# Kernel tuning notes

Measured on AMD Instinct MI355X. Metric: run time of the kernel, lower is better.

Reference implementation:

```python
import jax, jax.numpy as jnp
import numpy as np

C = 256      # edge_width
H = 8        # num_heads
D = C // H   # dot dim per head
SCALE = D ** (-0.5)
LN_EPS = 1e-5


def layernorm(x, g, b):
    mu = jnp.mean(x, axis=-1, keepdims=True)
    var = jnp.mean(jnp.square(x - mu), axis=-1, keepdims=True)
    return (x - mu) * jax.lax.rsqrt(var + LN_EPS) * g + b


def setup_inputs() -> dict:
    key = jax.random.key(0)
    ks = jax.random.split(key, 12)
    B, N = 1, 160
    s = 0.02
    return {
        "e": jax.random.normal(ks[0], (B, N, N, C), jnp.float32),
        "mask": jnp.zeros((B, N, N, H), jnp.float32),
        "ln_g": jnp.ones((C,), jnp.float32),
        "ln_b": jnp.zeros((C,), jnp.float32),
        "Wqkv_in": jax.random.normal(ks[1], (C, 3 * C), jnp.float32) * s,
        "bqkv_in": jnp.zeros((3 * C,), jnp.float32),
        "Weg_in": jax.random.normal(ks[2], (C, 2 * H), jnp.float32) * s,
        "beg_in": jnp.zeros((2 * H,), jnp.float32),
        "Wqkv_out": jax.random.normal(ks[3], (C, 3 * C), jnp.float32) * s,
        "bqkv_out": jnp.zeros((3 * C,), jnp.float32),
        "Weg_out": jax.random.normal(ks[4], (C, 2 * H), jnp.float32) * s,
        "beg_out": jnp.zeros((2 * H,), jnp.float32),
        "Wo": jax.random.normal(ks[5], (2 * C, C), jnp.float32) * s,
        "bo": jnp.zeros((C,), jnp.float32),
    }


def reference(e, mask, ln_g, ln_b, Wqkv_in, bqkv_in, Weg_in, beg_in,
              Wqkv_out, bqkv_out, Weg_out, beg_out, Wo, bo):
    B, N, _, _ = e.shape
    e_ln = layernorm(e, ln_g, ln_b)

    def split_qkv(W, b):
        qkv = e_ln @ W + b                       # [B,N,N,3C]
        q, k, v = jnp.split(qkv, 3, axis=-1)
        shp = (B, N, N, D, H)                    # (dot_dim, heads) heads fastest
        return q.reshape(shp) * SCALE, k.reshape(shp), v.reshape(shp)

    # ---- incoming triangle attention ----
    Q_in, K_in, V_in = split_qkv(Wqkv_in, bqkv_in)
    eg_in = (e_ln @ Weg_in + beg_in)[:, :, None, :, :]   # [B,N,1,N,2H]
    E_in, G_in = jnp.split(eg_in, 2, axis=-1)            # each [B,N,1,N,H]
    mask_in = mask[:, :, None]                           # [B,N,1,N,H]
    H_in = jnp.einsum('bijdh,bjkdh->bijkh', Q_in, K_in) + E_in
    A_in = jax.nn.softmax(H_in + mask_in, axis=3) * jax.nn.sigmoid(G_in + mask_in)
    Va_in = jnp.einsum('bijkh,bjkdh->bijdh', A_in, V_in)

    # ---- outgoing triangle attention ----
    Q_out, K_out, V_out = split_qkv(Wqkv_out, bqkv_out)
    eg_out = (e_ln @ Weg_out + beg_out)[:, :, :, None, :]  # [B,N,N,1,2H]
    E_out, G_out = jnp.split(eg_out, 2, axis=-1)           # each [B,N,N,1,H]
    mask_out = mask[:, :, :, None]                         # [B,N,N,1,H]
    H_out = jnp.einsum('bijdh,bkjdh->bkijh', Q_out, K_out) + E_out
    A_out = jax.nn.softmax(H_out + mask_out, axis=1) * jax.nn.sigmoid(G_out + mask_out)
    Va_out = jnp.einsum('bkijh,bkjdh->bijdh', A_out, V_out)

    Va = jnp.concatenate([Va_in, Va_out], axis=-1).reshape(B, N, N, 2 * C)
    return Va @ Wo + bo
```

## Files before the change

### kernel.cpp

```cpp
#include <hip/hip_runtime.h>

#define NDIM 160
#define MROWS (NDIM*NDIM)
#define NC1 1600
#define QK_SCALE 0.17677669529663687f
#define PSW 168

typedef __attribute__((ext_vector_type(8))) short bhalf8;
typedef __attribute__((ext_vector_type(4))) short short4v;
typedef __attribute__((ext_vector_type(4))) unsigned short ushort4v;
typedef __attribute__((ext_vector_type(4))) float floatx4;

static __device__ __forceinline__ short f2bf(float f) {
  unsigned int u = __builtin_bit_cast(unsigned int, f);
  u = (u + 0x7FFFu + ((u >> 16) & 1u)) >> 16;
  return (short)(u & 0xFFFFu);
}
static __device__ __forceinline__ float bf2f(unsigned short u) {
  return __builtin_bit_cast(float, ((unsigned int)u) << 16);
}
static __device__ __forceinline__ void gload_lds16(const short* g, short* l) {
  __builtin_amdgcn_global_load_lds(
      (const __attribute__((address_space(1))) void*)g,
      (__attribute__((address_space(3))) void*)l, 16, 0, 0);
}

__global__ __launch_bounds__(256) void prep_kernel(
    const float* __restrict__ Wqkv_in, const float* __restrict__ bqkv_in,
    const float* __restrict__ Weg_in, const float* __restrict__ beg_in,
    const float* __restrict__ Wqkv_out, const float* __restrict__ bqkv_out,
    const float* __restrict__ Weg_out, const float* __restrict__ beg_out,
    const float* __restrict__ Wo,
    short* __restrict__ WcT, float* __restrict__ biasc, short* __restrict__ WoT) {
  int idx = blockIdx.x * 256 + threadIdx.x;
  if (idx < NC1 * 256) {
    int n = idx >> 8, k = idx & 255;
    float w = 0.f;
    if (n < 768)        { w = Wqkv_in[k*768 + n];          if (n < 256) w *= QK_SCALE; }
    else if (n < 1536)  { int cc = n - 768; w = Wqkv_out[k*768 + cc]; if (cc < 256) w *= QK_SCALE; }
    else if (n < 1552)  { w = Weg_in[k*16 + (n - 1536)]; }
    else if (n < 1568)  { w = Weg_out[k*16 + (n - 1552)]; }
    WcT[n*256 + k] = f2bf(w);
    if (k == 0) {
      float bb = 0.f;
      if (n < 768)        { bb = bqkv_in[n];           if (n < 256) bb *= QK_SCALE; }
      else if (n < 1536)  { int cc = n - 768; bb = bqkv_out[cc]; if (cc < 256) bb *= QK_SCALE; }
      else if (n < 1552)  bb = beg_in[n - 1536];
      else if (n < 1568)  bb = beg_out[n - 1552];
      biasc[n] = bb;
    }
  } else {
    int i2 = idx - NC1 * 256;
    int c = i2 >> 9, cc = i2 & 511;
    int ch = (cc & 31) * 16 + (cc >> 5);
    WoT[c*512 + cc] = f2bf(Wo[ch*256 + c]);
  }
}

__global__ __launch_bounds__(256) void ln_kernel(
    const float* __restrict__ e, const float* __restrict__ g,
    const float* __restrict__ b, short* __restrict__ eln) {
  int row = blockIdx.x * 4 + (threadIdx.x >> 6);
  int lane = threadIdx.x & 63;
  float4 x = ((const float4*)(e + row*256))[lane];
  float s = x.x + x.y + x.z + x.w;
#pragma unroll
  for (int o = 1; o < 64; o <<= 1) s += __shfl_xor(s, o, 64);
  float mu = s * (1.f/256.f);
  float dx0 = x.x - mu, dx1 = x.y - mu, dx2 = x.z - mu, dx3 = x.w - mu;
  float q = dx0*dx0 + dx1*dx1 + dx2*dx2 + dx3*dx3;
#pragma unroll
  for (int o = 1; o < 64; o <<= 1) q += __shfl_xor(q, o, 64);
  float rstd = rsqrtf(q * (1.f/256.f) + 1e-5f);
  float4 gg = ((const float4*)g)[lane];
  float4 bb = ((const float4*)b)[lane];
  short4v y;
  y[0] = f2bf(dx0 * rstd * gg.x + bb.x);
  y[1] = f2bf(dx1 * rstd * gg.y + bb.y);
  y[2] = f2bf(dx2 * rstd * gg.z + bb.z);
  y[3] = f2bf(dx3 * rstd * gg.w + bb.w);
  ((short4v*)(eln + row*256))[lane] = y;
}

template<int K>
static __device__ __forceinline__ void gemm128_mainloop(
    const short* __restrict__ A0, const short* __restrict__ B0,
    short* SMEM, floatx4 (&acc)[4][4]) {
  const int wave = threadIdx.x >> 6, lane = threadIdx.x & 63;
  const int lr = lane & 15, lg = lane >> 4;
  const int wr = wave >> 1, wc = wave & 1;
  const int srow = (lane >> 2);
  const int scol = (lane & 3) * 8;
  constexpr int NSTEP = K / 32;

  auto stage = [&](int bsel, int s) {
#pragma unroll
    for (int q = 0; q < 2; q++) {
      int rbase = wave*32 + q*16;
      const short* ga = A0 + (rbase + srow)*K + s*32 + scol;
      short* la = SMEM + bsel*4096 + rbase*32;
      gload_lds16(ga, la);
      const short* gb = B0 + (rbase + srow)*K + s*32 + scol;
      short* lb = SMEM + 8192 + bsel*4096 + rbase*32;
      gload_lds16(gb, lb);
    }
  };

  stage(0, 0);
  __syncthreads();
  int bsel = 0;
  for (int s = 0; s < NSTEP; s++) {
    if (s + 1 < NSTEP) stage(bsel ^ 1, s + 1);
    bhalf8 af[4], bf[4];
#pragma unroll
    for (int mi = 0; mi < 4; mi++)
      af[mi] = *(const bhalf8*)(SMEM + bsel*4096 + (wr*64 + mi*16 + lr)*32 + lg*8);
#pragma unroll
    for (int ni = 0; ni < 4; ni++)
      bf[ni] = *(const bhalf8*)(SMEM + 8192 + bsel*4096 + (wc*64 + ni*16 + lr)*32 + lg*8);
#pragma unroll
    for (int mi = 0; mi < 4; mi++)
#pragma unroll
      for (int ni = 0; ni < 4; ni++)
        acc[mi][ni] = __builtin_amdgcn_mfma_f32_16x16x32_bf16(af[mi], bf[ni], acc[mi][ni], 0, 0, 0);
    __syncthreads();
    bsel ^= 1;
  }
}

__global__ __launch_bounds__(256) void qkv_gemm128_kernel(
    const short* __restrict__ eln, const short* __restrict__ WcT,
    const float* __restrict__ biasc,
    short* __restrict__ Qin, short* __restrict__ Kin, short* __restrict__ Vin,
    short* __restrict__ Qout, short* __restrict__ Kout) {
  int nt = blockIdx.x, mt = blockIdx.y;
  int part = nt >> 1;
  int n0 = part*256 + (nt & 1)*128;
  int m0 = mt * 128;
  __shared__ short SMEM[16384];
  floatx4 acc[4][4] = {};
  gemm128_mainloop<256>(eln + (size_t)m0*256, WcT + (size_t)n0*256, SMEM, acc);

  int wave = threadIdx.x >> 6, lane = threadIdx.x & 63;
  int lr = lane & 15, lg = lane >> 4;
  int wr = wave >> 1, wc = wave & 1;
  short (*T)[264] = (short(*)[264])SMEM;
#pragma unroll
  for (int c = 0; c < 4; c++) {
    __syncthreads();
    if (wr == (c >> 1)) {
#pragma unroll
      for (int i = 0; i < 2; i++) {
        int mi = (c & 1)*2 + i;
#pragma unroll
        for (int ni = 0; ni < 4; ni++)
#pragma unroll
          for (int r = 0; r < 4; r++) {
            int mm = i*16 + lg*4 + r;
            int nn = wc*64 + ni*16 + lr;
            T[mm][nn] = f2bf(acc[mi][ni][r] + biasc[n0 + nn]);
          }
      }
    }
    __syncthreads();
    int m0h = m0 + c*32;
    int ai = m0h / 160, bj0 = m0h % 160;
    if (part == 2) {
      int c2 = threadIdx.x & 127, half = threadIdx.x >> 7;
      int pcol = (nt & 1)*128 + c2;
      int d = pcol >> 3, h = pcol & 7;
      short vals[16];
#pragma unroll
      for (int m = 0; m < 16; m++) vals[m] = T[half*16 + m][c2];
      short* dst = Vin + ((size_t)(ai*8 + h)*32 + d)*160 + bj0 + half*16;
#pragma unroll
      for (int q = 0; q < 2; q++) *(bhalf8*)(dst + q*8) = *(const bhalf8*)(vals + q*8);
    } else {
      int m = threadIdx.x >> 3, h = threadIdx.x & 7;
      int bj = bj0 + m;
      short vals[16];
#pragma unroll
      for (int dd = 0; dd < 16; dd++) vals[dd] = T[m][h + dd*8];
      int d0 = (nt & 1) * 16;
      short* dst;
      if (part == 0)      dst = Qin  + ((size_t)(bj*8 + h)*160 + ai)*32 + d0;
      else if (part == 1) dst = Kin  + ((size_t)(ai*8 + h)*160 + bj)*32 + d0;
      else if (part == 3) dst = Qout + ((size_t)(bj*8 + h)*160 + ai)*32 + d0;
      else                dst = Kout + ((size_t)(bj*8 + h)*160 + ai)*32 + d0;
#pragma unroll
      for (int q = 0; q < 2; q++) *(bhalf8*)(dst + q*8) = *(const bhalf8*)(vals + q*8);
    }
  }
}

__global__ __launch_bounds__(256) void voutEG_kernel(
    const short* __restrict__ eln, const short* __restrict__ WcT,
    const float* __restrict__ biasc,
    short* __restrict__ Vout,
    float* __restrict__ Ein, float* __restrict__ Gin,
    float* __restrict__ Eout, float* __restrict__ Gout) {
  int wave = threadIdx.x >> 6, lane = threadIdx.x & 63;
  int lr = lane & 15, lg = lane >> 4;
  __shared__ short T[32][264];

  if (blockIdx.x == 0) {
    int n2 = blockIdx.y / 5; int bn1 = (blockIdx.y % 5) * 32;
    int m0 = bn1*160 + n2;
    const short* a0p = eln + (m0 + lr*160) * 256;
    const short* a1p = eln + (m0 + (16 + lr)*160) * 256;
    int nb = 5 * 256;
    int wn = nb + wave * 64;
    const short* b0p = WcT + (wn + lr) * 256;
    floatx4 acc[2][4] = {};
    for (int kk = 0; kk < 256; kk += 32) {
      int ko = kk + lg*8;
      bhalf8 a0 = *(const bhalf8*)(a0p + ko);
      bhalf8 a1 = *(const bhalf8*)(a1p + ko);
#pragma unroll
      for (int f = 0; f < 4; f++) {
        bhalf8 b = *(const bhalf8*)(b0p + f*16*256 + ko);
        acc[0][f] = __builtin_amdgcn_mfma_f32_16x16x32_bf16(a0, b, acc[0][f], 0, 0, 0);
        acc[1][f] = __builtin_amdgcn_mfma_f32_16x16x32_bf16(a1, b, acc[1][f], 0, 0, 0);
      }
    }
#pragma unroll
    for (int i = 0; i < 2; i++)
#pragma unroll
      for (int f = 0; f < 4; f++)
#pragma unroll
        for (int r = 0; r < 4; r++) {
          int mm = i*16 + lg*4 + r;
          int nn = wave*64 + f*16 + lr;
          T[mm][nn] = f2bf(acc[i][f][r] + biasc[nb + nn]);
        }
    __syncthreads();
    int c = threadIdx.x, h = c & 7, d = c >> 3;
    short vals[32];
#pragma unroll
    for (int m = 0; m < 32; m++) vals[m] = T[m][c];
    short* dst = Vout + ((size_t)(n2*8 + h)*32 + d)*160 + bn1;
#pragma unroll
    for (int q = 0; q < 4; q++) *(bhalf8*)(dst + q*8) = *(const bhalf8*)(vals + q*8);
  } else {
    int m0 = blockIdx.y * 32;
    int wn = 1536 + wave * 16;
    const short* a0p = eln + (m0 + lr) * 256;
    const short* a1p = eln + (m0 + 16 + lr) * 256;
    const short* b0p = WcT + (wn + lr) * 256;
    floatx4 acc[2] = {};
    for (int kk = 0; kk < 256; kk += 32) {
      int ko = kk + lg*8;
      bhalf8 a0 = *(const bhalf8*)(a0p + ko);
      bhalf8 a1 = *(const bhalf8*)(a1p + ko);
      bhalf8 b  = *(const bhalf8*)(b0p + ko);
      acc[0] = __builtin_amdgcn_mfma_f32_16x16x32_bf16(a0, b, acc[0], 0, 0, 0);
      acc[1] = __builtin_amdgcn_mfma_f32_16x16x32_bf16(a1, b, acc[1], 0, 0, 0);
    }
    int n = wn + lr;
    if (n < 1568) {
      int t = n - 1536;
      float* dst = (t < 8) ? Ein : (t < 16) ? Gin : (t < 24) ? Eout : Gout;
#pragma unroll
      for (int i = 0; i < 2; i++)
#pragma unroll
        for (int r = 0; r < 4; r++) {
          int m = m0 + i*16 + lg*4 + r;
          dst[m*8 + (t & 7)] = acc[i][r] + biasc[n];
        }
    }
  }
}

__global__ __launch_bounds__(256) void ems_kernel(
    const float* __restrict__ Ein, const float* __restrict__ Gin,
    const float* __restrict__ Eout, const float* __restrict__ Gout,
    const float* __restrict__ mask,
    unsigned short* __restrict__ EMS, unsigned short* __restrict__ GSS) {
  int idx = blockIdx.x * 256 + threadIdx.x;
  if (idx >= 16 * 25600) return;
  int hb = idx / 25600;
  int rem = idx - hb * 25600;
  int i = rem / 160, k = rem - i * 160;
  int br = hb >> 3, h = hb & 7;
  int src = br ? ((k*160 + i)*8 + h) : ((i*160 + k)*8 + h);
  float ev = br ? Eout[src] : Ein[src];
  float gv = br ? Gout[src] : Gin[src];
  float mv = mask[src];
  EMS[idx] = (unsigned short)f2bf(ev + mv);
  GSS[idx] = (unsigned short)f2bf(1.f / (1.f + __expf(-(gv + mv))));
}

__global__ __launch_bounds__(256) void attn_kernel(
    const short* __restrict__ Qin, const short* __restrict__ Kin, const short* __restrict__ Vin,
    const short* __restrict__ Qout, const short* __restrict__ Kout, const short* __restrict__ Vout,
    const unsigned short* __restrict__ EMS, const unsigned short* __restrict__ GSS,
    short* __restrict__ Va) {
  int wave = threadIdx.x >> 6, lane = threadIdx.x & 63;
  int g = blockIdx.x * 4 + wave;
  int pair = g % 5;
  int u = g / 5;
  int h = u & 7;
  int v = u >> 3;
  int br = v & 1;
  int j = v >> 1;
  int lr = lane & 15, lg = lane >> 4;
  const short* Qg = (br ? Qout : Qin) + (j*8 + h) * 5120;
  const short* Kg = (br ? Kout : Kin) + (j*8 + h) * 5120;
  const short* Vg = (br ? Vout : Vin) + (j*8 + h) * 5120;
  const unsigned short* EMh = EMS + (br*8 + h) * 25600;
  const unsigned short* GSh = GSS + (br*8 + h) * 25600;
  __shared__ short Ps[4][16][PSW];

  bhalf8 kf[10];
#pragma unroll
  for (int kt = 0; kt < 10; kt++)
    kf[kt] = *(const bhalf8*)(Kg + (kt*16 + lr)*32 + lg*8);

  const floatx4 zero = {0.f, 0.f, 0.f, 0.f};
  int hh = br*8 + h;
#pragma unroll
  for (int qi = 0; qi < 2; qi++) {
    int qt = pair*2 + qi;
    int i0 = qt*16;
    bhalf8 qf = *(const bhalf8*)(Qg + (i0 + lr)*32 + lg*8);
    int erow = (i0 + lr)*160;
    floatx4 s[10];
#pragma unroll
    for (int kt = 0; kt < 10; kt++) {
      ushort4v em = *(const ushort4v*)(EMh + erow + kt*16 + lg*4);
      floatx4 c0;
      c0[0] = bf2f(em[0]); c0[1] = bf2f(em[1]); c0[2] = bf2f(em[2]); c0[3] = bf2f(em[3]);
      s[kt] = __builtin_amdgcn_mfma_f32_16x16x32_bf16(kf[kt], qf, c0, 0, 0, 0);
    }
    float mx = -1e30f;
#pragma unroll
    for (int kt = 0; kt < 10; kt++)
#pragma unroll
      for (int r = 0; r < 4; r++) mx = fmaxf(mx, s[kt][r]);
    mx = fmaxf(mx, __shfl_xor(mx, 16, 64));
    mx = fmaxf(mx, __shfl_xor(mx, 32, 64));
    float sm = 0.f;
#pragma unroll
    for (int kt = 0; kt < 10; kt++)
#pragma unroll
      for (int r = 0; r < 4; r++) {
        float p = __expf(s[kt][r] - mx);
        s[kt][r] = p;
        sm += p;
      }
    sm += __shfl_xor(sm, 16, 64);
    sm += __shfl_xor(sm, 32, 64);
    float rs = 1.f / sm;
#pragma unroll
    for (int kt = 0; kt < 10; kt++) {
      ushort4v gs = *(const ushort4v*)(GSh + erow + kt*16 + lg*4);
      short4v pk;
      pk[0] = f2bf(s[kt][0] * rs * bf2f(gs[0]));
      pk[1] = f2bf(s[kt][1] * rs * bf2f(gs[1]));
      pk[2] = f2bf(s[kt][2] * rs * bf2f(gs[2]));
      pk[3] = f2bf(s[kt][3] * rs * bf2f(gs[3]));
      *(short4v*)(&Ps[wave][lr][kt*16 + lg*4]) = pk;
    }
    floatx4 accv0 = zero, accv1 = zero;
#pragma unroll
    for (int kc = 0; kc < 5; kc++) {
      bhalf8 ap  = *(const bhalf8*)(&Ps[wave][lr][kc*32 + lg*8]);
      bhalf8 bv0 = *(const bhalf8*)(Vg + lr*160 + kc*32 + lg*8);
      bhalf8 bv1 = *(const bhalf8*)(Vg + (16 + lr)*160 + kc*32 + lg*8);
      accv0 = __builtin_amdgcn_mfma_f32_16x16x32_bf16(ap, bv0, accv0, 0, 0, 0);
      accv1 = __builtin_amdgcn_mfma_f32_16x16x32_bf16(ap, bv1, accv1, 0, 0, 0);
    }
#pragma unroll
    for (int r = 0; r < 4; r++) {
      int i = i0 + lg*4 + r;
      short* vp = Va + ((size_t)i*160 + j)*512 + hh*32;
      vp[lr]      = f2bf(accv0[r]);
      vp[16 + lr] = f2bf(accv1[r]);
    }
  }
}

__global__ __launch_bounds__(256) void out_gemm128_kernel(
    const short* __restrict__ Va, const short* __restrict__ WoT,
    const float* __restrict__ bo, float* __restrict__ out) {
  int n0 = blockIdx.x * 128, m0 = blockIdx.y * 128;
  __shared__ short SMEM[16384];
  floatx4 acc[4][4] = {};
  gemm128_mainloop<512>(Va + (size_t)m0*512, WoT + (size_t)n0*512, SMEM, acc);
  int wave = threadIdx.x >> 6, lane = threadIdx.x & 63;
  int lr = lane & 15, lg = lane >> 4;
  int wr = wave >> 1, wc = wave & 1;
#pragma unroll
  for (int mi = 0; mi < 4; mi++)
#pragma unroll
    for (int ni = 0; ni < 4; ni++)
#pragma unroll
      for (int r = 0; r < 4; r++) {
        int m = m0 + wr*64 + mi*16 + lg*4 + r;
        int n = n0 + wc*64 + ni*16 + lr;
        out[(size_t)m*256 + n] = acc[mi][ni][r] + bo[n];
      }
}

extern "C" void kernel_launch(void* const* d_in, const int* in_sizes, int n_in,
                              void* d_out, int out_size, void* d_ws, size_t ws_size,
                              hipStream_t stream) {
  const float* e        = (const float*)d_in[0];
  const float* mask     = (const float*)d_in[1];
  const float* ln_g     = (const float*)d_in[2];
  const float* ln_b     = (const float*)d_in[3];
  const float* Wqkv_in  = (const float*)d_in[4];
  const float* bqkv_in  = (const float*)d_in[5];
  const float* Weg_in   = (const float*)d_in[6];
  const float* beg_in   = (const float*)d_in[7];
  const float* Wqkv_out = (const float*)d_in[8];
  const float* bqkv_out = (const float*)d_in[9];
  const float* Weg_out  = (const float*)d_in[10];
  const float* beg_out  = (const float*)d_in[11];
  const float* Wo       = (const float*)d_in[12];
  const float* bo       = (const float*)d_in[13];
  float* out = (float*)d_out;

  char* ws = (char*)d_ws;
  size_t off = 0;
  auto alloc = [&](size_t bytes) -> void* {
    void* p = ws + off;
    off += (bytes + 255) & ~(size_t)255;
    return p;
  };
  short* eln   = (short*)alloc((size_t)MROWS*256*2);
  short* WcT   = (short*)alloc((size_t)NC1*256*2);
  float* biasc = (float*)alloc((size_t)NC1*4);
  short* WoT   = (short*)alloc((size_t)256*512*2);
  short* Qin   = (short*)alloc((size_t)160*8*160*32*2);
  short* Kin   = (short*)alloc((size_t)160*8*160*32*2);
  short* Vin   = (short*)alloc((size_t)160*8*160*32*2);
  short* Qout  = (short*)alloc((size_t)160*8*160*32*2);
  short* Kout  = (short*)alloc((size_t)160*8*160*32*2);
  short* Vout  = (short*)alloc((size_t)160*8*160*32*2);
  float* Ein   = (float*)alloc((size_t)160*160*8*4);
  float* Gin   = (float*)alloc((size_t)160*160*8*4);
  float* Eout  = (float*)alloc((size_t)160*160*8*4);
  float* Gout  = (float*)alloc((size_t)160*160*8*4);
  unsigned short* EMS = (unsigned short*)alloc((size_t)16*25600*2);
  unsigned short* GSS = (unsigned short*)alloc((size_t)16*25600*2);
  short* Vabuf = (short*)alloc((size_t)MROWS*512*2);

  prep_kernel<<<2112, 256, 0, stream>>>(Wqkv_in, bqkv_in, Weg_in, beg_in,
                                        Wqkv_out, bqkv_out, Weg_out, beg_out,
                                        Wo, WcT, biasc, WoT);
  ln_kernel<<<6400, 256, 0, stream>>>(e, ln_g, ln_b, eln);
  qkv_gemm128_kernel<<<dim3(10, 200), 256, 0, stream>>>(eln, WcT, biasc,
      Qin, Kin, Vin, Qout, Kout);
  voutEG_kernel<<<dim3(2, 800), 256, 0, stream>>>(eln, WcT, biasc,
      Vout, Ein, Gin, Eout, Gout);
  ems_kernel<<<1600, 256, 0, stream>>>(Ein, Gin, Eout, Gout, mask, EMS, GSS);
  attn_kernel<<<3200, 256, 0, stream>>>(Qin, Kin, Vin, Qout, Kout, Vout,
      EMS, GSS, Vabuf);
  out_gemm128_kernel<<<dim3(2, 200), 256, 0, stream>>>(Vabuf, WoT, bo, out);
}
```

Before: 284.8 us.

## Drop softmax max pass, defer normalization, and vectorize attention output stores

The attention kernel now exponentiates scores directly, without subtracting the row max. It fuses exp, gating and the P write into the QK loop and applies the 1/sum normalization after the PV matmul. The PV MFMA operands are swapped so each lane holds contiguous output elements, which allows 4-wide short stores instead of scalar stores. This cuts register pressure (launch bounds raised to 4 blocks per SM) and removes two passes over the scores. The cost is a risk of exp overflow when scores are large.

New measurement: 291.4 us. 1.02x slower.

```diff
diff --git a/kernel.cpp b/kernel.cpp
--- a/kernel.cpp
+++ b/kernel.cpp
@@ -290,7 +290,7 @@
   GSS[idx] = (unsigned short)f2bf(1.f / (1.f + __expf(-(gv + mv))));
 }
 
-__global__ __launch_bounds__(256) void attn_kernel(
+__global__ __launch_bounds__(256, 4) void attn_kernel(
     const short* __restrict__ Qin, const short* __restrict__ Kin, const short* __restrict__ Vin,
     const short* __restrict__ Qout, const short* __restrict__ Kout, const short* __restrict__ Vout,
     const unsigned short* __restrict__ EMS, const unsigned short* __restrict__ GSS,
@@ -324,59 +324,44 @@
     int i0 = qt*16;
     bhalf8 qf = *(const bhalf8*)(Qg + (i0 + lr)*32 + lg*8);
     int erow = (i0 + lr)*160;
-    floatx4 s[10];
+    float sum = 0.f;
 #pragma unroll
     for (int kt = 0; kt < 10; kt++) {
       ushort4v em = *(const ushort4v*)(EMh + erow + kt*16 + lg*4);
       floatx4 c0;
       c0[0] = bf2f(em[0]); c0[1] = bf2f(em[1]); c0[2] = bf2f(em[2]); c0[3] = bf2f(em[3]);
-      s[kt] = __builtin_amdgcn_mfma_f32_16x16x32_bf16(kf[kt], qf, c0, 0, 0, 0);
-    }
-    float mx = -1e30f;
-#pragma unroll
-    for (int kt = 0; kt < 10; kt++)
-#pragma unroll
-      for (int r = 0; r < 4; r++) mx = fmaxf(mx, s[kt][r]);
-    mx = fmaxf(mx, __shfl_xor(mx, 16, 64));
-    mx = fmaxf(mx, __shfl_xor(mx, 32, 64));
-    float sm = 0.f;
-#pragma unroll
-    for (int kt = 0; kt < 10; kt++)
-#pragma unroll
-      for (int r = 0; r < 4; r++) {
-        float p = __expf(s[kt][r] - mx);
-        s[kt][r] = p;
-        sm += p;
-      }
-    sm += __shfl_xor(sm, 16, 64);
-    sm += __shfl_xor(sm, 32, 64);
-    float rs = 1.f / sm;
-#pragma unroll
-    for (int kt = 0; kt < 10; kt++) {
+      floatx4 s = __builtin_amdgcn_mfma_f32_16x16x32_bf16(kf[kt], qf, c0, 0, 0, 0);
       ushort4v gs = *(const ushort4v*)(GSh + erow + kt*16 + lg*4);
+      float p0 = __expf(s[0]), p1 = __expf(s[1]), p2 = __expf(s[2]), p3 = __expf(s[3]);
+      sum += (p0 + p1) + (p2 + p3);
       short4v pk;
-      pk[0] = f2bf(s[kt][0] * rs * bf2f(gs[0]));
-      pk[1] = f2bf(s[kt][1] * rs * bf2f(gs[1]));
-      pk[2] = f2bf(s[kt][2] * rs * bf2f(gs[2]));
-      pk[3] = f2bf(s[kt][3] * rs * bf2f(gs[3]));
+      pk[0] = f2bf(p0 * bf2f(gs[0]));
+      pk[1] = f2bf(p1 * bf2f(gs[1]));
+      pk[2] = f2bf(p2 * bf2f(gs[2]));
+      pk[3] = f2bf(p3 * bf2f(gs[3]));
       *(short4v*)(&Ps[wave][lr][kt*16 + lg*4]) = pk;
     }
-    floatx4 accv0 = zero, accv1 = zero;
+    sum += __shfl_xor(sum, 16, 64);
+    sum += __shfl_xor(sum, 32, 64);
+    float rs = 1.f / sum;
+    floatx4 acc0 = zero, acc1 = zero;
 #pragma unroll
     for (int kc = 0; kc < 5; kc++) {
       bhalf8 ap  = *(const bhalf8*)(&Ps[wave][lr][kc*32 + lg*8]);
       bhalf8 bv0 = *(const bhalf8*)(Vg + lr*160 + kc*32 + lg*8);
       bhalf8 bv1 = *(const bhalf8*)(Vg + (16 + lr)*160 + kc*32 + lg*8);
-      accv0 = __builtin_amdgcn_mfma_f32_16x16x32_bf16(ap, bv0, accv0, 0, 0, 0);
-      accv1 = __builtin_amdgcn_mfma_f32_16x16x32_bf16(ap, bv1, accv1, 0, 0, 0);
-    }
+      acc0 = __builtin_amdgcn_mfma_f32_16x16x32_bf16(bv0, ap, acc0, 0, 0, 0);
+      acc1 = __builtin_amdgcn_mfma_f32_16x16x32_bf16(bv1, ap, acc1, 0, 0, 0);
+    }
+    short* vp = Va + ((size_t)(i0 + lr)*160 + j)*512 + hh*32;
+    short4v o0, o1;
 #pragma unroll
     for (int r = 0; r < 4; r++) {
-      int i = i0 + lg*4 + r;
-      short* vp = Va + ((size_t)i*160 + j)*512 + hh*32;
-      vp[lr]      = f2bf(accv0[r]);
-      vp[16 + lr] = f2bf(accv1[r]);
-    }
+      o0[r] = f2bf(acc0[r] * rs);
+      o1[r] = f2bf(acc1[r] * rs);
+    }
+    *(short4v*)(vp + lg*4) = o0;
+    *(short4v*)(vp + 16 + lg*4) = o1;
   }
 }
 
```
